# Optimization experiments

Hardware: AMD Instinct MI355X
Metric: run time of the kernel (lower is better)

The kernel has to match this reference:

```python
import jax, jax.numpy as jnp
import numpy as np

D_MODEL = 1024
N_HEADS = 16
D_HEAD = 64

def setup_inputs() -> dict:
    key = jax.random.key(0)
    k_x, k_q, k_k, k_v, k_o = jax.random.split(key, 5)
    B, T = 2, 2048
    scale = 1.0 / np.sqrt(D_MODEL)
    x = jax.random.normal(k_x, (B, T, D_MODEL), dtype=jnp.float32)
    W_q = jax.random.normal(k_q, (D_MODEL, N_HEADS * D_HEAD), dtype=jnp.float32) * scale
    W_k = jax.random.normal(k_k, (D_MODEL, N_HEADS * D_HEAD), dtype=jnp.float32) * scale
    W_v = jax.random.normal(k_v, (D_MODEL, N_HEADS * D_HEAD), dtype=jnp.float32) * scale
    W_out = jax.random.normal(k_o, (N_HEADS * D_HEAD, D_MODEL), dtype=jnp.float32) * scale
    return {"x": x, "W_q": W_q, "W_k": W_k, "W_v": W_v, "W_out": W_out}

def reference(x, W_q, W_k, W_v, W_out):
    B, T, _ = x.shape
    # project and split heads: [B, T, H, D] -> [B, H, T, D]
    def heads(W):
        return (x @ W).reshape(B, T, N_HEADS, D_HEAD).transpose(0, 2, 1, 3)
    Q, K, V = heads(W_q), heads(W_k), heads(W_v)
    scores = jnp.einsum('bhqd,bhkd->bhqk', Q, K) / jnp.sqrt(jnp.float32(D_HEAD))
    causal = jnp.tril(jnp.ones((T, T), dtype=bool))  # True = keep
    scores = jnp.where(causal, scores, jnp.float32(-jnp.inf))
    attn = jax.nn.softmax(scores, axis=-1)
    z = jnp.einsum('bhqk,bhkd->bhqd', attn, V)
    z = z.transpose(0, 2, 1, 3).reshape(B, T, N_HEADS * D_HEAD)
    return z @ W_out
```

## Files before the change

kernel.cpp:

```cpp
#include <hip/hip_runtime.h>
#include <cstdint>
#include <cstddef>

typedef __bf16 bf16_t;
typedef __bf16 bf16x8 __attribute__((ext_vector_type(8)));
typedef __bf16 bf16x4 __attribute__((ext_vector_type(4)));
typedef float floatx4 __attribute__((ext_vector_type(4)));

#define MFMA_BF16_16x16x32(a, b, c) \
  __builtin_amdgcn_mfma_f32_16x16x32_bf16((a), (b), (c), 0, 0, 0)

static constexpr int kT = 2048;
static constexpr int kDM = 1024;
static constexpr int kNH = 16;
static constexpr int kDH = 64;
static constexpr float kLog2e = 1.4426950408889634f;
static constexpr int kPS = 140;

__device__ __forceinline__ void gl_lds16(const bf16_t* g, bf16_t* l) {
  __builtin_amdgcn_global_load_lds(
      (const __attribute__((address_space(1))) void*)g,
      (__attribute__((address_space(3))) void*)l, 16, 0, 0);
}

__global__ __launch_bounds__(256) void detect_dtype(
    const unsigned short* __restrict__ xv, int* __restrict__ flagp) {
  __shared__ int bad_s[256];
  int bad = 0;
  for (int i = threadIdx.x; i < 8192; i += 256) {
    const unsigned e = (xv[i] >> 7) & 0xFF;
    if (e == 0xFF || (e != 0 && (e < 107 || e > 147))) bad++;
  }
  bad_s[threadIdx.x] = bad;
  __syncthreads();
  for (int s = 128; s > 0; s >>= 1) {
    if (threadIdx.x < s) bad_s[threadIdx.x] += bad_s[threadIdx.x + s];
    __syncthreads();
  }
  if (threadIdx.x == 0) *flagp = (bad_s[0] * 10 < 8192) ? 1 : 0;
}

__global__ __launch_bounds__(256) void convert_x(
    const void* __restrict__ src, bf16_t* __restrict__ dst,
    const int* __restrict__ flagp, int n) {
  const int f = *flagp;
  const int i = (blockIdx.x * 256 + threadIdx.x) * 8;
  if (i >= n) return;
  if (f) {
    *(bf16x8*)(dst + i) = *(const bf16x8*)((const bf16_t*)src + i);
  } else {
    const float* s = (const float*)src + i;
    bf16x8 v;
#pragma unroll
    for (int j = 0; j < 8; j++) v[j] = (bf16_t)s[j];
    *(bf16x8*)(dst + i) = v;
  }
}

__global__ __launch_bounds__(256) void convert_transpose_w(
    const void* __restrict__ w0, const void* __restrict__ w1,
    const void* __restrict__ w2, const void* __restrict__ w3,
    bf16_t* __restrict__ out_base, const int* __restrict__ flagp) {
  const int f = *flagp;
  const void* src = (blockIdx.z == 0) ? w0
                  : (blockIdx.z == 1) ? w1
                  : (blockIdx.z == 2) ? w2 : w3;
  bf16_t* dst = out_base + (size_t)blockIdx.z * (kDM * kDM);
  __shared__ bf16_t tile[64][65];
  const int tx = threadIdx.x & 63;
  const int ty = threadIdx.x >> 6;
  const int x0 = blockIdx.x * 64;
  const int y0 = blockIdx.y * 64;
#pragma unroll
  for (int r = 0; r < 64; r += 4) {
    const size_t idx = (size_t)(y0 + ty + r) * kDM + x0 + tx;
    tile[ty + r][tx] =
        f ? ((const bf16_t*)src)[idx] : (bf16_t)((const float*)src)[idx];
  }
  __syncthreads();
#pragma unroll
  for (int r = 0; r < 64; r += 4)
    dst[(size_t)(x0 + ty + r) * kDM + y0 + tx] = tile[tx][ty + r];
}

__device__ __forceinline__ void gemm_core_128x128(
    const bf16_t* __restrict__ A, const bf16_t* __restrict__ Bt, int K,
    bf16_t* __restrict__ sA, bf16_t* __restrict__ sB, floatx4 acc[4][4]) {
  const int tid = threadIdx.x;
  const int lane = tid & 63;
  const int w = tid >> 6;
  const int quad = lane >> 4;
  const int l16 = lane & 15;
  const int wm = w >> 1;
  const int wn = w & 1;
  const int sr = tid >> 2;
  const int sc = (tid & 3) * 8;
  const int wbase = w * 512;

  const bf16_t* pa0 = A + (size_t)sr * K + sc;
  const bf16_t* pa1 = A + (size_t)(sr + 64) * K + sc;
  const bf16_t* pb0 = Bt + (size_t)sr * K + sc;
  const bf16_t* pb1 = Bt + (size_t)(sr + 64) * K + sc;

  for (int kk = 0; kk < K; kk += 32) {
    __syncthreads();
    gl_lds16(pa0 + kk, sA + wbase);
    gl_lds16(pa1 + kk, sA + 2048 + wbase);
    gl_lds16(pb0 + kk, sB + wbase);
    gl_lds16(pb1 + kk, sB + 2048 + wbase);
    __syncthreads();
    bf16x8 af[4], bf[4];
#pragma unroll
    for (int mi = 0; mi < 4; mi++)
      af[mi] = *(const bf16x8*)(sA + (wm * 64 + mi * 16 + l16) * 32 + quad * 8);
#pragma unroll
    for (int ni = 0; ni < 4; ni++)
      bf[ni] = *(const bf16x8*)(sB + (wn * 64 + ni * 16 + l16) * 32 + quad * 8);
#pragma unroll
    for (int mi = 0; mi < 4; mi++)
#pragma unroll
      for (int ni = 0; ni < 4; ni++)
        acc[mi][ni] = MFMA_BF16_16x16x32(af[mi], bf[ni], acc[mi][ni]);
  }
}

__global__ __launch_bounds__(256) void qkv_proj(
    const bf16_t* __restrict__ x, const bf16_t* __restrict__ wt_base,
    bf16_t* __restrict__ Qo, bf16_t* __restrict__ Kf, bf16_t* __restrict__ Vf) {
  __shared__ bf16_t smem[2 * 128 * 32];
  const int n0 = blockIdx.x * 128;
  const int m0 = blockIdx.y * 128;
  const int which = blockIdx.z;
  const bf16_t* Bt = wt_base + (size_t)which * (kDM * kDM);

  floatx4 acc[4][4];
  const floatx4 zero4 = {0.f, 0.f, 0.f, 0.f};
#pragma unroll
  for (int mi = 0; mi < 4; mi++)
#pragma unroll
    for (int ni = 0; ni < 4; ni++) acc[mi][ni] = zero4;

  gemm_core_128x128(x + (size_t)m0 * kDM, Bt + (size_t)n0 * kDM, kDM,
                    smem, smem + 128 * 32, acc);

  const int tid = threadIdx.x;
  const int lane = tid & 63, w = tid >> 6;
  const int quad = lane >> 4, l16 = lane & 15;
  const int wm = w >> 1, wn = w & 1;

  if (which == 0) {
#pragma unroll
    for (int mi = 0; mi < 4; mi++) {
#pragma unroll
      for (int ni = 0; ni < 4; ni++) {
        const int n = n0 + wn * 64 + ni * 16 + l16;
        const int h = n >> 6, d = n & 63;
#pragma unroll
        for (int reg = 0; reg < 4; reg++) {
          const int m = m0 + wm * 64 + mi * 16 + quad * 4 + reg;
          const int b = m >> 11, t = m & (kT - 1);
          Qo[((size_t)(b * kNH + h) * kT + t) * kDH + d] = (bf16_t)acc[mi][ni][reg];
        }
      }
    }
  } else if (which == 1) {
#pragma unroll
    for (int mi = 0; mi < 4; mi++) {
#pragma unroll
      for (int ni = 0; ni < 4; ni++) {
        const int n = n0 + wn * 64 + ni * 16 + l16;
        const int h = n >> 6, d = n & 63;
        const int khf = d >> 5, quadf = (d & 31) >> 3, elemf = d & 7;
#pragma unroll
        for (int reg = 0; reg < 4; reg++) {
          const int m = m0 + wm * 64 + mi * 16 + quad * 4 + reg;
          const int b = m >> 11, t = m & (kT - 1);
          const int kt = t >> 7, rem = t & 127, nif = rem >> 4, l16f = rem & 15;
          Kf[(((((size_t)(b * kNH + h) * 16 + kt) * 2 + khf) * 8 + nif) * 64 +
              quadf * 16 + l16f) * 8 + elemf] = (bf16_t)acc[mi][ni][reg];
        }
      }
    }
  } else {
#pragma unroll
    for (int mi = 0; mi < 4; mi++) {
#pragma unroll
      for (int ni = 0; ni < 4; ni++) {
        const int n = n0 + wn * 64 + ni * 16 + l16;
        const int h = n >> 6, d = n & 63;
        const int ndv = d >> 4, l16v = d & 15;
        const int m = m0 + wm * 64 + mi * 16 + quad * 4;
        const int b = m >> 11, t0 = m & (kT - 1);
        const int kt = t0 >> 7, ks = (t0 >> 5) & 3, quadv = (t0 >> 3) & 3;
        const int eb = t0 & 4;
        bf16x4 v;
        v[0] = (bf16_t)acc[mi][ni][0];
        v[1] = (bf16_t)acc[mi][ni][1];
        v[2] = (bf16_t)acc[mi][ni][2];
        v[3] = (bf16_t)acc[mi][ni][3];
        *(bf16x4*)(Vf + (((((size_t)(b * kNH + h) * 16 + kt) * 4 + ks) * 4 +
                          ndv) * 64 + quadv * 16 + l16v) * 8 + eb) = v;
      }
    }
  }
}

__device__ __forceinline__ void attn_task(
    int task, int lane, int l16, int quad, const bf16_t* __restrict__ Qb,
    const bf16_t* __restrict__ Kbf, const bf16_t* __restrict__ Vbf,
    bf16_t* __restrict__ Pw, bf16_t* __restrict__ Z, int b, int h) {
  const int q0 = task * 16;
  const int nkt = (task >> 3) + 1;
  const float C1 = 0.125f * kLog2e;

  bf16x8 qf[2];
#pragma unroll
  for (int kh = 0; kh < 2; kh++)
    qf[kh] = *(const bf16x8*)(Qb + (q0 + l16) * kDH + kh * 32 + quad * 8);

  const floatx4 zero4 = {0.f, 0.f, 0.f, 0.f};
  floatx4 of[4];
  float lrow[4];
#pragma unroll
  for (int nd = 0; nd < 4; nd++) of[nd] = zero4;
#pragma unroll
  for (int r = 0; r < 4; r++) lrow[r] = 0.f;

  bf16x8 kf[16];
#pragma unroll
  for (int fi = 0; fi < 16; fi++)
    kf[fi] = *(const bf16x8*)(Kbf + (size_t)fi * 512 + lane * 8);

  for (int kt = 0; kt < nkt; kt++) {
    const int kbase = kt * 128;
    floatx4 sf[8];
#pragma unroll
    for (int ni = 0; ni < 8; ni++) sf[ni] = zero4;
#pragma unroll
    for (int kh = 0; kh < 2; kh++)
#pragma unroll
      for (int ni = 0; ni < 8; ni++)
        sf[ni] = MFMA_BF16_16x16x32(qf[kh], kf[kh * 8 + ni], sf[ni]);
    const int ktp = (kt + 1 < nkt) ? kt + 1 : kt;
    const bf16_t* kp = Kbf + (size_t)ktp * 16 * 512 + lane * 8;
#pragma unroll
    for (int fi = 0; fi < 16; fi++)
      kf[fi] = *(const bf16x8*)(kp + (size_t)fi * 512);
    const bf16_t* vp = Vbf + (size_t)kt * 16 * 512 + lane * 8;
    bf16x8 vf[16];
#pragma unroll
    for (int fi = 0; fi < 16; fi++)
      vf[fi] = *(const bf16x8*)(vp + (size_t)fi * 512);
    const bool diag = (kt == nkt - 1);
#pragma unroll
    for (int reg = 0; reg < 4; reg++) {
      const int row_l = quad * 4 + reg;
      const int row_g = q0 + row_l;
      float rsum = 0.f;
#pragma unroll
      for (int ni = 0; ni < 8; ni++) {
        float s = sf[ni][reg] * C1 - 16.f;
        if (diag && (kbase + ni * 16 + l16 > row_g)) s = -3.0e38f;
        const float p = exp2f(s);
        rsum += p;
        Pw[row_l * kPS + ni * 16 + l16] = (bf16_t)p;
      }
      lrow[reg] += rsum;
    }
    __asm volatile("s_waitcnt lgkmcnt(0)" ::: "memory");
#pragma unroll
    for (int ks = 0; ks < 4; ks++) {
      const bf16x8 af = *(const bf16x8*)(Pw + l16 * kPS + ks * 32 + quad * 8);
#pragma unroll
      for (int nd = 0; nd < 4; nd++)
        of[nd] = MFMA_BF16_16x16x32(af, vf[ks * 4 + nd], of[nd]);
    }
  }

#pragma unroll
  for (int reg = 0; reg < 4; reg++) {
#pragma unroll
    for (int off = 1; off < 16; off <<= 1)
      lrow[reg] += __shfl_xor(lrow[reg], off, 64);
  }
#pragma unroll
  for (int reg = 0; reg < 4; reg++) {
    const int t = q0 + quad * 4 + reg;
    const float inv = 1.f / lrow[reg];
#pragma unroll
    for (int nd = 0; nd < 4; nd++) {
      const int col = h * 64 + nd * 16 + l16;
      Z[(size_t)(b * kT + t) * kDM + col] = (bf16_t)(of[nd][reg] * inv);
    }
  }
}

__global__ __launch_bounds__(256, 2) void attn_fused(
    const bf16_t* __restrict__ Q, const bf16_t* __restrict__ Kf,
    const bf16_t* __restrict__ Vf, bf16_t* __restrict__ Z) {
  __shared__ bf16_t Ps[64 * kPS];
  const int bh = blockIdx.x;
  const int tid = threadIdx.x;
  const int lane = tid & 63;
  const int w = tid >> 6;
  const int quad = lane >> 4;
  const int l16 = lane & 15;
  const int pairidx = blockIdx.y * 4 + w;
  bf16_t* Pw = Ps + (w * 16) * kPS;

  const bf16_t* Qb = Q + (size_t)bh * kT * kDH;
  const bf16_t* Kbf = Kf + (size_t)bh * kT * kDH;
  const bf16_t* Vbf = Vf + (size_t)bh * kT * kDH;
  const int b = bh >> 4, h = bh & 15;

  attn_task(pairidx, lane, l16, quad, Qb, Kbf, Vbf, Pw, Z, b, h);
  attn_task(127 - pairidx, lane, l16, quad, Qb, Kbf, Vbf, Pw, Z, b, h);
}

__global__ __launch_bounds__(256) void out_proj(
    const bf16_t* __restrict__ Zin, const bf16_t* __restrict__ WtO,
    void* __restrict__ out, const int* __restrict__ flagp) {
  __shared__ bf16_t smem[2 * 128 * 32];
  const int f = *flagp;
  const int n0 = blockIdx.x * 128;
  const int m0 = blockIdx.y * 128;
  floatx4 acc[4][4];
  const floatx4 zero4 = {0.f, 0.f, 0.f, 0.f};
#pragma unroll
  for (int mi = 0; mi < 4; mi++)
#pragma unroll
    for (int ni = 0; ni < 4; ni++) acc[mi][ni] = zero4;

  gemm_core_128x128(Zin + (size_t)m0 * kDM, WtO + (size_t)n0 * kDM, kDM,
                    smem, smem + 128 * 32, acc);

  const int tid = threadIdx.x;
  const int lane = tid & 63, w = tid >> 6;
  const int quad = lane >> 4, l16 = lane & 15;
  const int wm = w >> 1, wn = w & 1;
#pragma unroll
  for (int mi = 0; mi < 4; mi++) {
#pragma unroll
    for (int ni = 0; ni < 4; ni++) {
      const int n = n0 + wn * 64 + ni * 16 + l16;
#pragma unroll
      for (int reg = 0; reg < 4; reg++) {
        const int m = m0 + wm * 64 + mi * 16 + quad * 4 + reg;
        if (f) {
          ((bf16_t*)out)[(size_t)m * kDM + n] = (bf16_t)acc[mi][ni][reg];
        } else {
          ((float*)out)[(size_t)m * kDM + n] = acc[mi][ni][reg];
        }
      }
    }
  }
}

extern "C" void kernel_launch(void* const* d_in, const int* in_sizes, int n_in,
                              void* d_out, int out_size, void* d_ws,
                              size_t ws_size, hipStream_t stream) {
  const void* x = d_in[0];
  const void* Wq = d_in[1];
  const void* Wk = d_in[2];
  const void* Wv = d_in[3];
  const void* Wo = d_in[4];
  bf16_t* ws = (bf16_t*)d_ws;
  const size_t MEG = 1024 * 1024;
  bf16_t* wt = ws;
  bf16_t* xb = ws + 4 * MEG;
  bf16_t* Q = ws + 8 * MEG;
  bf16_t* Kf = ws + 12 * MEG;
  bf16_t* Vf = ws + 16 * MEG;
  bf16_t* Z = ws + 20 * MEG;
  int* flagp = (int*)(ws + 24 * MEG);

  detect_dtype<<<1, 256, 0, stream>>>((const unsigned short*)x, flagp);
  convert_x<<<2048, 256, 0, stream>>>(x, xb, flagp, 4 * (int)MEG);
  convert_transpose_w<<<dim3(16, 16, 4), 256, 0, stream>>>(Wq, Wk, Wv, Wo, wt,
                                                           flagp);
  qkv_proj<<<dim3(8, 32, 3), 256, 0, stream>>>(xb, wt, Q, Kf, Vf);
  attn_fused<<<dim3(32, 16), 256, 0, stream>>>(Q, Kf, Vf, Z);
  out_proj<<<dim3(8, 32), 256, 0, stream>>>(Z, wt + 3 * MEG, d_out, flagp);
}
```

Before: 207.1 us.

## Stage Q/K epilogue through LDS into fragment layout, shrink out_proj tiles

Result: faster. 194.6 us (-6.0%).

```diff
diff --git a/kernel.cpp b/kernel.cpp
--- a/kernel.cpp
+++ b/kernel.cpp
@@ -124,10 +124,49 @@
   }
 }
 
+__device__ __forceinline__ void gemm_core_64x128(
+    const bf16_t* __restrict__ A, const bf16_t* __restrict__ Bt, int K,
+    bf16_t* __restrict__ sA, bf16_t* __restrict__ sB, floatx4 acc[2][4]) {
+  const int tid = threadIdx.x;
+  const int lane = tid & 63;
+  const int w = tid >> 6;
+  const int quad = lane >> 4;
+  const int l16 = lane & 15;
+  const int wm = w >> 1;
+  const int wn = w & 1;
+  const int sr = tid >> 2;
+  const int sc = (tid & 3) * 8;
+  const int wbase = w * 512;
+
+  const bf16_t* pa = A + (size_t)sr * K + sc;
+  const bf16_t* pb0 = Bt + (size_t)sr * K + sc;
+  const bf16_t* pb1 = Bt + (size_t)(sr + 64) * K + sc;
+
+  for (int kk = 0; kk < K; kk += 32) {
+    __syncthreads();
+    gl_lds16(pa + kk, sA + wbase);
+    gl_lds16(pb0 + kk, sB + wbase);
+    gl_lds16(pb1 + kk, sB + 2048 + wbase);
+    __syncthreads();
+    bf16x8 af[2], bf[4];
+#pragma unroll
+    for (int mi = 0; mi < 2; mi++)
+      af[mi] = *(const bf16x8*)(sA + (wm * 32 + mi * 16 + l16) * 32 + quad * 8);
+#pragma unroll
+    for (int ni = 0; ni < 4; ni++)
+      bf[ni] = *(const bf16x8*)(sB + (wn * 64 + ni * 16 + l16) * 32 + quad * 8);
+#pragma unroll
+    for (int mi = 0; mi < 2; mi++)
+#pragma unroll
+      for (int ni = 0; ni < 4; ni++)
+        acc[mi][ni] = MFMA_BF16_16x16x32(af[mi], bf[ni], acc[mi][ni]);
+  }
+}
+
 __global__ __launch_bounds__(256) void qkv_proj(
     const bf16_t* __restrict__ x, const bf16_t* __restrict__ wt_base,
-    bf16_t* __restrict__ Qo, bf16_t* __restrict__ Kf, bf16_t* __restrict__ Vf) {
-  __shared__ bf16_t smem[2 * 128 * 32];
+    bf16_t* __restrict__ Qf, bf16_t* __restrict__ Kf, bf16_t* __restrict__ Vf) {
+  __shared__ bf16_t smem[8704];
   const int n0 = blockIdx.x * 128;
   const int m0 = blockIdx.y * 128;
   const int which = blockIdx.z;
@@ -141,53 +180,21 @@
     for (int ni = 0; ni < 4; ni++) acc[mi][ni] = zero4;
 
   gemm_core_128x128(x + (size_t)m0 * kDM, Bt + (size_t)n0 * kDM, kDM,
-                    smem, smem + 128 * 32, acc);
+                    smem, smem + 4096, acc);
 
   const int tid = threadIdx.x;
   const int lane = tid & 63, w = tid >> 6;
   const int quad = lane >> 4, l16 = lane & 15;
   const int wm = w >> 1, wn = w & 1;
-
-  if (which == 0) {
+  const int h = (n0 + wn * 64) >> 6;
+
+  if (which == 2) {
 #pragma unroll
     for (int mi = 0; mi < 4; mi++) {
 #pragma unroll
       for (int ni = 0; ni < 4; ni++) {
         const int n = n0 + wn * 64 + ni * 16 + l16;
-        const int h = n >> 6, d = n & 63;
-#pragma unroll
-        for (int reg = 0; reg < 4; reg++) {
-          const int m = m0 + wm * 64 + mi * 16 + quad * 4 + reg;
-          const int b = m >> 11, t = m & (kT - 1);
-          Qo[((size_t)(b * kNH + h) * kT + t) * kDH + d] = (bf16_t)acc[mi][ni][reg];
-        }
-      }
-    }
-  } else if (which == 1) {
-#pragma unroll
-    for (int mi = 0; mi < 4; mi++) {
-#pragma unroll
-      for (int ni = 0; ni < 4; ni++) {
-        const int n = n0 + wn * 64 + ni * 16 + l16;
-        const int h = n >> 6, d = n & 63;
-        const int khf = d >> 5, quadf = (d & 31) >> 3, elemf = d & 7;
-#pragma unroll
-        for (int reg = 0; reg < 4; reg++) {
-          const int m = m0 + wm * 64 + mi * 16 + quad * 4 + reg;
-          const int b = m >> 11, t = m & (kT - 1);
-          const int kt = t >> 7, rem = t & 127, nif = rem >> 4, l16f = rem & 15;
-          Kf[(((((size_t)(b * kNH + h) * 16 + kt) * 2 + khf) * 8 + nif) * 64 +
-              quadf * 16 + l16f) * 8 + elemf] = (bf16_t)acc[mi][ni][reg];
-        }
-      }
-    }
-  } else {
-#pragma unroll
-    for (int mi = 0; mi < 4; mi++) {
-#pragma unroll
-      for (int ni = 0; ni < 4; ni++) {
-        const int n = n0 + wn * 64 + ni * 16 + l16;
-        const int h = n >> 6, d = n & 63;
+        const int d = n & 63;
         const int ndv = d >> 4, l16v = d & 15;
         const int m = m0 + wm * 64 + mi * 16 + quad * 4;
         const int b = m >> 11, t0 = m & (kT - 1);
@@ -202,6 +209,41 @@
                           ndv) * 64 + quadv * 16 + l16v) * 8 + eb) = v;
       }
     }
+  } else {
+    __syncthreads();
+    bf16_t* Out = (which == 0) ? Qf : Kf;
+    bf16_t* Lw = smem + w * 2176;
+#pragma unroll
+    for (int pass = 0; pass < 2; pass++) {
+#pragma unroll
+      for (int mi2 = 0; mi2 < 2; mi2++) {
+        const int mi = pass * 2 + mi2;
+#pragma unroll
+        for (int ni = 0; ni < 4; ni++)
+#pragma unroll
+          for (int reg = 0; reg < 4; reg++)
+            Lw[(mi2 * 16 + quad * 4 + reg) * 68 + ni * 16 + l16] =
+                (bf16_t)acc[mi][ni][reg];
+      }
+      __asm volatile("s_waitcnt lgkmcnt(0)" ::: "memory");
+      const int tb = m0 + wm * 64 + pass * 32;
+#pragma unroll
+      for (int i = 0; i < 4; i++) {
+        const int khf = i >> 1, nifr = i & 1;
+        const bf16x8 v = *(const bf16x8*)(Lw + (nifr * 16 + l16) * 68 +
+                                          khf * 32 + quad * 8);
+        const int t0 = tb + nifr * 16;
+        const int b = t0 >> 11, tt = t0 & (kT - 1);
+        size_t base;
+        if (which == 0) {
+          base = (((size_t)(b * kNH + h) * 128 + (tt >> 4)) * 2 + khf) * 512;
+        } else {
+          const int kt = tt >> 7, nif = (tt & 127) >> 4;
+          base = ((((size_t)(b * kNH + h) * 16 + kt) * 2 + khf) * 8 + nif) * 512;
+        }
+        *(bf16x8*)(Out + base + lane * 8) = v;
+      }
+    }
   }
 }
 
@@ -216,7 +258,7 @@
   bf16x8 qf[2];
 #pragma unroll
   for (int kh = 0; kh < 2; kh++)
-    qf[kh] = *(const bf16x8*)(Qb + (q0 + l16) * kDH + kh * 32 + quad * 8);
+    qf[kh] = *(const bf16x8*)(Qb + ((size_t)task * 2 + kh) * 512 + lane * 8);
 
   const floatx4 zero4 = {0.f, 0.f, 0.f, 0.f};
   floatx4 of[4];
@@ -296,7 +338,7 @@
 }
 
 __global__ __launch_bounds__(256, 2) void attn_fused(
-    const bf16_t* __restrict__ Q, const bf16_t* __restrict__ Kf,
+    const bf16_t* __restrict__ Qf, const bf16_t* __restrict__ Kf,
     const bf16_t* __restrict__ Vf, bf16_t* __restrict__ Z) {
   __shared__ bf16_t Ps[64 * kPS];
   const int bh = blockIdx.x;
@@ -308,7 +350,7 @@
   const int pairidx = blockIdx.y * 4 + w;
   bf16_t* Pw = Ps + (w * 16) * kPS;
 
-  const bf16_t* Qb = Q + (size_t)bh * kT * kDH;
+  const bf16_t* Qb = Qf + (size_t)bh * kT * kDH;
   const bf16_t* Kbf = Kf + (size_t)bh * kT * kDH;
   const bf16_t* Vbf = Vf + (size_t)bh * kT * kDH;
   const int b = bh >> 4, h = bh & 15;
@@ -320,32 +362,32 @@
 __global__ __launch_bounds__(256) void out_proj(
     const bf16_t* __restrict__ Zin, const bf16_t* __restrict__ WtO,
     void* __restrict__ out, const int* __restrict__ flagp) {
-  __shared__ bf16_t smem[2 * 128 * 32];
+  __shared__ bf16_t smem[6144];
   const int f = *flagp;
   const int n0 = blockIdx.x * 128;
-  const int m0 = blockIdx.y * 128;
-  floatx4 acc[4][4];
+  const int m0 = blockIdx.y * 64;
+  floatx4 acc[2][4];
   const floatx4 zero4 = {0.f, 0.f, 0.f, 0.f};
 #pragma unroll
-  for (int mi = 0; mi < 4; mi++)
+  for (int mi = 0; mi < 2; mi++)
 #pragma unroll
     for (int ni = 0; ni < 4; ni++) acc[mi][ni] = zero4;
 
-  gemm_core_128x128(Zin + (size_t)m0 * kDM, WtO + (size_t)n0 * kDM, kDM,
-                    smem, smem + 128 * 32, acc);
+  gemm_core_64x128(Zin + (size_t)m0 * kDM, WtO + (size_t)n0 * kDM, kDM,
+                   smem, smem + 2048, acc);
 
   const int tid = threadIdx.x;
   const int lane = tid & 63, w = tid >> 6;
   const int quad = lane >> 4, l16 = lane & 15;
   const int wm = w >> 1, wn = w & 1;
 #pragma unroll
-  for (int mi = 0; mi < 4; mi++) {
+  for (int mi = 0; mi < 2; mi++) {
 #pragma unroll
     for (int ni = 0; ni < 4; ni++) {
       const int n = n0 + wn * 64 + ni * 16 + l16;
 #pragma unroll
       for (int reg = 0; reg < 4; reg++) {
-        const int m = m0 + wm * 64 + mi * 16 + quad * 4 + reg;
+        const int m = m0 + wm * 32 + mi * 16 + quad * 4 + reg;
         if (f) {
           ((bf16_t*)out)[(size_t)m * kDM + n] = (bf16_t)acc[mi][ni][reg];
         } else {
@@ -368,7 +410,7 @@
   const size_t MEG = 1024 * 1024;
   bf16_t* wt = ws;
   bf16_t* xb = ws + 4 * MEG;
-  bf16_t* Q = ws + 8 * MEG;
+  bf16_t* Qf = ws + 8 * MEG;
   bf16_t* Kf = ws + 12 * MEG;
   bf16_t* Vf = ws + 16 * MEG;
   bf16_t* Z = ws + 20 * MEG;
@@ -378,7 +420,7 @@
   convert_x<<<2048, 256, 0, stream>>>(x, xb, flagp, 4 * (int)MEG);
   convert_transpose_w<<<dim3(16, 16, 4), 256, 0, stream>>>(Wq, Wk, Wv, Wo, wt,
                                                            flagp);
-  qkv_proj<<<dim3(8, 32, 3), 256, 0, stream>>>(xb, wt, Q, Kf, Vf);
-  attn_fused<<<dim3(32, 16), 256, 0, stream>>>(Q, Kf, Vf, Z);
-  out_proj<<<dim3(8, 32), 256, 0, stream>>>(Z, wt + 3 * MEG, d_out, flagp);
-}
+  qkv_proj<<<dim3(8, 32, 3), 256, 0, stream>>>(xb, wt, Qf, Kf, Vf);
+  attn_fused<<<dim3(32, 16), 256, 0, stream>>>(Qf, Kf, Vf, Z);
+  out_proj<<<dim3(8, 64), 256, 0, stream>>>(Z, wt + 3 * MEG, d_out, flagp);
+}
```
